# Optimization experiments

Measured on AMD Instinct MI355X. Metric: run time of the kernel, lower is better.

Reference implementation:

```python
import jax, jax.numpy as jnp
import numpy as np

H, W, HID = 7, 7, 512
IN_DIM = 1024

def _grid_edges(h, w):
    e = []
    for r in range(h):
        for c in range(w):
            n = r * w + c
            if c < w - 1:
                e.append((n, n + 1))
            if r < h - 1:
                e.append((n, n + w))
    return np.asarray(e, dtype=np.int32).T  # [2, 84]

_BASE = _grid_edges(H, W)

def setup_inputs() -> dict:
    key = jax.random.key(0)
    ks = jax.random.split(key, 16)
    B = 1024
    s = 0.02
    return {
        "visual_feat": jax.random.normal(ks[0], (B, 512, H, W), jnp.float32),
        "tactile_feat": jax.random.normal(ks[1], (B, 512, H, W), jnp.float32),
        "proj_W": jax.random.normal(ks[2], (IN_DIM, 2), jnp.float32) * s,
        "proj_b": jnp.zeros((2,), jnp.float32),
        "gc1_rel_W": jax.random.normal(ks[3], (IN_DIM, HID), jnp.float32) * s,
        "gc1_rel_b": jnp.zeros((HID,), jnp.float32),
        "gc1_root_W": jax.random.normal(ks[4], (IN_DIM, HID), jnp.float32) * s,
        "bn1_gamma": jnp.ones((HID,), jnp.float32),
        "bn1_beta": jnp.zeros((HID,), jnp.float32),
        "gc2_rel_W": jax.random.normal(ks[5], (HID, HID), jnp.float32) * s,
        "gc2_rel_b": jnp.zeros((HID,), jnp.float32),
        "gc2_root_W": jax.random.normal(ks[6], (HID, HID), jnp.float32) * s,
        "bn2_gamma": jnp.ones((HID,), jnp.float32),
        "bn2_beta": jnp.zeros((HID,), jnp.float32),
        "dec_W": jax.random.normal(ks[7], (HID + 1, HID), jnp.float32) * s,
        "dec_b": jnp.zeros((HID,), jnp.float32),
    }

def _batched_edges(B):
    off = (np.arange(B, dtype=np.int32) * (H * W))[:, None]
    src = (_BASE[0][None, :] + off).reshape(-1)
    dst = (_BASE[1][None, :] + off).reshape(-1)
    return jnp.asarray(src), jnp.asarray(dst)

def _bn(x, gamma, beta):
    mu = x.mean(0)
    var = x.var(0)  # biased, matches torch BN normalization
    return (x - mu) * jax.lax.rsqrt(var + 1e-5) * gamma + beta

def _graph_conv(x, src, dst, ew, W_rel, b_rel, W_root, N):
    msg = ew[:, None] * x[src]                      # [E, D]
    agg = jax.ops.segment_sum(msg, dst, num_segments=N)
    deg = jax.ops.segment_sum(jnp.ones_like(ew), dst, num_segments=N)
    agg = agg / jnp.maximum(deg, 1.0)[:, None]
    return agg @ W_rel + b_rel + x @ W_root

def reference(visual_feat, tactile_feat, proj_W, proj_b,
              gc1_rel_W, gc1_rel_b, gc1_root_W, bn1_gamma, bn1_beta,
              gc2_rel_W, gc2_rel_b, gc2_root_W, bn2_gamma, bn2_beta,
              dec_W, dec_b):
    B = visual_feat.shape[0]
    N = B * H * W
    # node features: concat channels, NCHW -> N x (2C)
    node = jnp.concatenate([visual_feat, tactile_feat], axis=1)
    node = node.transpose(0, 2, 3, 1).reshape(N, IN_DIM)
    src, dst = _batched_edges(B)
    coords = node @ proj_W + proj_b                 # [N, 2]
    dist = jnp.linalg.norm(coords[src] - coords[dst], axis=1)
    edge_attr = jax.nn.sigmoid(1.0 / (dist + 1e-6))  # [E]
    alpha = jnp.exp(edge_attr)
    alpha = alpha / (alpha.sum() + 1e-8)            # global normalization over all edges
    x = jax.nn.relu(_bn(_graph_conv(node, src, dst, alpha, gc1_rel_W, gc1_rel_b, gc1_root_W, N), bn1_gamma, bn1_beta))
    x = jax.nn.relu(_bn(_graph_conv(x, src, dst, alpha, gc2_rel_W, gc2_rel_b, gc2_root_W, N), bn2_gamma, bn2_beta))
    # scatter_mean of edge_attr over both endpoints
    ids = jnp.concatenate([src, dst])
    vals = jnp.concatenate([edge_attr, edge_attr])
    nw_sum = jax.ops.segment_sum(vals, ids, num_segments=N)
    nw_cnt = jax.ops.segment_sum(jnp.ones_like(vals), ids, num_segments=N)
    node_w = nw_sum / jnp.maximum(nw_cnt, 1.0)      # [N]
    x = jax.nn.relu(jnp.concatenate([x, node_w[:, None]], axis=1) @ dec_W + dec_b)
    return x.reshape(B, H, W, HID).transpose(0, 3, 1, 2)
```

## Files before the change

### kernel.cpp

```cpp
#include <hip/hip_runtime.h>
#include <hip/hip_bf16.h>

typedef float f32x4 __attribute__((ext_vector_type(4)));
typedef short s16x8 __attribute__((ext_vector_type(8)));

#define N_NODES 50176

static __device__ __forceinline__ ushort f2bf(float x) {
    __hip_bfloat16 h = __float2bfloat16(x);
    return *reinterpret_cast<ushort*>(&h);
}
static __device__ __forceinline__ float bf2f(ushort u) {
    __hip_bfloat16 h = *reinterpret_cast<__hip_bfloat16*>(&u);
    return __bfloat162float(h);
}

__global__ void k_prep(const float* W1r, const float* W1t, const float* W2r, const float* W2t,
                       const float* decW, ushort* Bt1, ushort* Bt2, ushort* Bt3, float* decLast,
                       float* alpha_sum, float* bn_acc) {
    int idx = blockIdx.x * 256 + threadIdx.x;
    if (idx < 512 * 2048) {
        int j = idx >> 11, k = idx & 2047;
        float v = (k < 1024) ? W1r[k * 512 + j] : W1t[(k - 1024) * 512 + j];
        Bt1[idx] = f2bf(v);
    }
    if (idx < 512 * 1024) {
        int j = idx >> 10, k = idx & 1023;
        float v = (k < 512) ? W2r[k * 512 + j] : W2t[(k - 512) * 512 + j];
        Bt2[idx] = f2bf(v);
    }
    if (idx < 512 * 512) {
        int j = idx >> 9, k = idx & 511;
        Bt3[idx] = f2bf(decW[k * 512 + j]);
    }
    if (idx < 512) decLast[idx] = decW[512 * 512 + idx];
    if (idx < 2048) bn_acc[idx] = 0.f;
    if (idx == 0) alpha_sum[0] = 0.f;
}

__global__ void k_transpose(const float* vis, const float* tac, ushort* xcat1) {
    int b = blockIdx.x, tid = threadIdx.x;
    __shared__ ushort tile[128 * 50];
    for (int chunk = 0; chunk < 8; ++chunk) {
        const float* src = (chunk < 4 ? vis : tac) + ((size_t)b * 512 + (chunk & 3) * 128) * 49;
        for (int p = tid; p < 128 * 49; p += 256) {
            int d = p / 49, n = p - d * 49;
            tile[d * 50 + n] = f2bf(src[p]);
        }
        __syncthreads();
        for (int p = tid; p < 49 * 128; p += 256) {
            int n = p >> 7, d = p & 127;
            xcat1[((size_t)(b * 49 + n)) * 2048 + 1024 + chunk * 128 + d] = tile[d * 50 + n];
        }
        __syncthreads();
    }
}

__global__ void k_coords(const ushort* xcat1, const float* projW, const float* projb, float* coords) {
    __shared__ float pw[2048];
    int tid = threadIdx.x;
    for (int p = tid; p < 2048; p += 256) pw[p] = projW[p];
    __syncthreads();
    int lane = tid & 63, wave = tid >> 6;
    int n = blockIdx.x * 4 + wave;
    const ushort* row = xcat1 + (size_t)n * 2048 + 1024;
    float c0 = 0.f, c1 = 0.f;
    for (int j = 0; j < 16; ++j) {
        int d = j * 64 + lane;
        float v = bf2f(row[d]);
        c0 += v * pw[2 * d];
        c1 += v * pw[2 * d + 1];
    }
    for (int off = 32; off; off >>= 1) { c0 += __shfl_down(c0, off); c1 += __shfl_down(c1, off); }
    if (lane == 0) { coords[2 * n] = c0 + projb[0]; coords[2 * n + 1] = c1 + projb[1]; }
}

__global__ void k_edges(const float* coords, float* ew_exp, float* node_w, float* alpha_sum) {
    int b = blockIdx.x, tid = threadIdx.x;
    __shared__ float cx[49], cy[49], ea[84];
    __shared__ float wsum[2];
    if (tid < 49) { cx[tid] = coords[(b * 49 + tid) * 2]; cy[tid] = coords[(b * 49 + tid) * 2 + 1]; }
    __syncthreads();
    float ex = 0.f;
    if (tid < 84) {
        int s, d2;
        if (tid < 42) { int r = tid / 6, c = tid - r * 6; s = r * 7 + c; d2 = s + 1; }
        else { int t = tid - 42; int r = t / 7, c = t - r * 7; s = r * 7 + c; d2 = s + 7; }
        float dx = cx[s] - cx[d2], dy = cy[s] - cy[d2];
        float dist = sqrtf(dx * dx + dy * dy);
        float attr = 1.f / (1.f + expf(-(1.f / (dist + 1e-6f))));
        ea[tid] = attr;
        ex = expf(attr);
        ew_exp[b * 84 + tid] = ex;
    }
    for (int off = 32; off; off >>= 1) ex += __shfl_down(ex, off);
    if ((tid & 63) == 0) wsum[tid >> 6] = ex;
    __syncthreads();
    if (tid == 0) atomicAdd(alpha_sum, wsum[0] + wsum[1]);
    if (tid < 49) {
        int r = tid / 7, c = tid - r * 7;
        float s = 0.f; int cnt = 0;
        if (c > 0) { s += ea[r * 6 + c - 1]; cnt++; }
        if (c < 6) { s += ea[r * 6 + c]; cnt++; }
        if (r > 0) { s += ea[42 + (r - 1) * 7 + c]; cnt++; }
        if (r < 6) { s += ea[42 + r * 7 + c]; cnt++; }
        node_w[b * 49 + tid] = s / (float)cnt;
    }
}

__global__ void k_aggin(ushort* __restrict__ xcat, const float* __restrict__ ew,
                        const float* __restrict__ asum) {
    int T = blockIdx.x * 256 + threadIdx.x;
    int n = T >> 7, ch = T & 7 * 16 + 15;
    ch = T & 127;
    int b = n / 49, sp = n - b * 49;
    int r = sp / 7, c = sp - r * 7;
    float acc[8];
#pragma unroll
    for (int k = 0; k < 8; ++k) acc[k] = 0.f;
    int deg = (c > 0) + (r > 0);
    if (deg) {
        float sc = (1.f / (asum[0] + 1e-8f)) / (float)deg;
        if (c > 0) {
            float wl = ew[b * 84 + r * 6 + (c - 1)] * sc;
            s16x8 lv = *(const s16x8*)(xcat + (size_t)(n - 1) * 2048 + 1024 + ch * 8);
#pragma unroll
            for (int k = 0; k < 8; ++k) acc[k] += wl * bf2f((ushort)lv[k]);
        }
        if (r > 0) {
            float wt = ew[b * 84 + 42 + (r - 1) * 7 + c] * sc;
            s16x8 tv = *(const s16x8*)(xcat + (size_t)(n - 7) * 2048 + 1024 + ch * 8);
#pragma unroll
            for (int k = 0; k < 8; ++k) acc[k] += wt * bf2f((ushort)tv[k]);
        }
    }
    s16x8 o;
#pragma unroll
    for (int k = 0; k < 8; ++k) o[k] = (short)f2bf(acc[k]);
    *(s16x8*)(xcat + (size_t)n * 2048 + ch * 8) = o;
}

template <int EPI>
__global__ __launch_bounds__(256, 2)
void k_gemm(const ushort* __restrict__ A, const ushort* __restrict__ Bt, float* __restrict__ C,
            int K,
            const float* __restrict__ bias, float* __restrict__ bn_sum, float* __restrict__ bn_sumsq,
            const float* __restrict__ node_w, const float* __restrict__ decLast,
            const float* __restrict__ decb, float* __restrict__ out) {
    __shared__ ushort As[128 * 40];
    __shared__ ushort Bs[128 * 40];
    const int rowb = blockIdx.x >> 2, colb = blockIdx.x & 3;
    const int row0 = rowb << 7, col0 = colb << 7;
    const int tid = threadIdx.x;
    const int lane = tid & 63, wave = tid >> 6;
    const int wm = (wave & 1) << 6, wn = (wave >> 1) << 6;
    const int quad = lane >> 4, l16 = lane & 15;
    const int K8 = K >> 3;

    const uint4* Ag = (const uint4*)A;
    const uint4* Bg = (const uint4*)Bt;
    uint4* As4 = (uint4*)As;
    uint4* Bs4 = (uint4*)Bs;

    const int r0s = tid >> 2, kc = tid & 3;
    const size_t ia0 = (size_t)(row0 + r0s) * K8 + kc;
    const size_t ia1 = (size_t)(row0 + r0s + 64) * K8 + kc;
    const size_t ib0 = (size_t)(col0 + r0s) * K8 + kc;
    const size_t ib1 = (size_t)(col0 + r0s + 64) * K8 + kc;
    const int sa0 = r0s * 5 + kc, sa1 = (r0s + 64) * 5 + kc;

    f32x4 acc[4][4];
#pragma unroll
    for (int i = 0; i < 4; ++i)
#pragma unroll
        for (int j = 0; j < 4; ++j) acc[i][j] = (f32x4)0.f;

    const int nk = K >> 5;
    uint4 a0 = Ag[ia0], a1 = Ag[ia1], b0 = Bg[ib0], b1 = Bg[ib1];
    for (int kt = 0; kt < nk; ++kt) {
        As4[sa0] = a0; As4[sa1] = a1; Bs4[sa0] = b0; Bs4[sa1] = b1;
        __syncthreads();
        if (kt + 1 < nk) {
            const size_t o = (size_t)(kt + 1) * 4;
            a0 = Ag[ia0 + o]; a1 = Ag[ia1 + o]; b0 = Bg[ib0 + o]; b1 = Bg[ib1 + o];
        }
        s16x8 af[4], bf[4];
#pragma unroll
        for (int i = 0; i < 4; ++i) af[i] = *(const s16x8*)&As[(wm + i * 16 + l16) * 40 + quad * 8];
#pragma unroll
        for (int j = 0; j < 4; ++j) bf[j] = *(const s16x8*)&Bs[(wn + j * 16 + l16) * 40 + quad * 8];
#pragma unroll
        for (int i = 0; i < 4; ++i)
#pragma unroll
            for (int j = 0; j < 4; ++j)
                acc[i][j] = __builtin_amdgcn_mfma_f32_16x16x32_bf16(af[i], bf[j], acc[i][j], 0, 0, 0);
        __syncthreads();
    }

    if (EPI == 0) {
#pragma unroll
        for (int j = 0; j < 4; ++j) {
            int col = col0 + wn + j * 16 + l16;
            float bcol = bias[col];
            float s = 0.f, s2 = 0.f;
#pragma unroll
            for (int i = 0; i < 4; ++i) {
#pragma unroll
                for (int r = 0; r < 4; ++r) {
                    int m = row0 + wm + i * 16 + quad * 4 + r;
                    float v = acc[i][j][r] + bcol;
                    C[(size_t)m * 512 + col] = v;
                    s += v; s2 += v * v;
                }
            }
            s += __shfl_xor(s, 16); s += __shfl_xor(s, 32);
            s2 += __shfl_xor(s2, 16); s2 += __shfl_xor(s2, 32);
            if (quad == 0) { atomicAdd(&bn_sum[col], s); atomicAdd(&bn_sumsq[col], s2); }
        }
    } else {
#pragma unroll
        for (int i = 0; i < 4; ++i) {
#pragma unroll
            for (int j = 0; j < 4; ++j) {
#pragma unroll
                for (int r = 0; r < 4; ++r) {
                    int m = row0 + wm + i * 16 + quad * 4 + r;
                    int n = col0 + wn + j * 16 + l16;
                    float v = acc[i][j][r];
                    v += node_w[m] * decLast[n] + decb[n];
                    v = fmaxf(v, 0.f);
                    int bb = m / 49, sp = m - bb * 49;
                    out[((size_t)bb * 512 + n) * 49 + sp] = v;
                }
            }
        }
    }
}

__global__ void k_bnstat(const float* bn_sum, const float* bn_sumsq, const float* gamma, const float* beta,
                         float* scale, float* shift) {
    int d = threadIdx.x;
    const float invN = 1.f / (float)N_NODES;
    float mu = bn_sum[d] * invN;
    float var = bn_sumsq[d] * invN - mu * mu;
    float sc = gamma[d] * rsqrtf(var + 1e-5f);
    scale[d] = sc;
    shift[d] = beta[d] - mu * sc;
}

__global__ __launch_bounds__(256) void k_bnagg(const float* __restrict__ P, const float* __restrict__ ew,
                                               const float* __restrict__ asum,
                                               const float* __restrict__ scale, const float* __restrict__ shift,
                                               ushort* __restrict__ xcat) {
    int b = blockIdx.x, tid = threadIdx.x;
    __shared__ ushort xl[49 * 512];
    __shared__ float wl[49], wt[49];
    if (tid < 49) {
        int r = tid / 7, c = tid - r * 7;
        int deg = (c > 0) + (r > 0);
        float sc = deg ? (1.f / (asum[0] + 1e-8f)) / (float)deg : 0.f;
        wl[tid] = (c > 0) ? ew[b * 84 + r * 6 + (c - 1)] * sc : 0.f;
        wt[tid] = (r > 0) ? ew[b * 84 + 42 + (r - 1) * 7 + c] * sc : 0.f;
    }
    int dc = tid & 127;
    int sp0 = tid >> 7;
    float4 scl = ((const float4*)scale)[dc];
    float4 shf = ((const float4*)shift)[dc];
    for (int sp = sp0; sp < 49; sp += 2) {
        float4 v = ((const float4*)(P + ((size_t)b * 49 + sp) * 512))[dc];
        ushort4 o;
        o.x = f2bf(fmaxf(v.x * scl.x + shf.x, 0.f));
        o.y = f2bf(fmaxf(v.y * scl.y + shf.y, 0.f));
        o.z = f2bf(fmaxf(v.z * scl.z + shf.z, 0.f));
        o.w = f2bf(fmaxf(v.w * scl.w + shf.w, 0.f));
        *(ushort4*)&xl[sp * 512 + dc * 4] = o;
        ((ushort4*)(xcat + ((size_t)b * 49 + sp) * 1024 + 512))[dc] = o;
    }
    __syncthreads();
    for (int sp = sp0; sp < 49; sp += 2) {
        float a0 = 0.f, a1 = 0.f, a2 = 0.f, a3 = 0.f;
        float w1 = wl[sp], w2 = wt[sp];
        if (w1 != 0.f) {
            ushort4 u = *(const ushort4*)&xl[(sp - 1) * 512 + dc * 4];
            a0 += w1 * bf2f(u.x); a1 += w1 * bf2f(u.y); a2 += w1 * bf2f(u.z); a3 += w1 * bf2f(u.w);
        }
        if (w2 != 0.f) {
            ushort4 u = *(const ushort4*)&xl[(sp - 7) * 512 + dc * 4];
            a0 += w2 * bf2f(u.x); a1 += w2 * bf2f(u.y); a2 += w2 * bf2f(u.z); a3 += w2 * bf2f(u.w);
        }
        ushort4 o;
        o.x = f2bf(a0); o.y = f2bf(a1); o.z = f2bf(a2); o.w = f2bf(a3);
        ((ushort4*)(xcat + ((size_t)b * 49 + sp) * 1024))[dc] = o;
    }
}

__global__ void k_bnapply(const float* __restrict__ x, const float* __restrict__ scale,
                          const float* __restrict__ shift, ushort* __restrict__ xb) {
    int tid = threadIdx.x;
    size_t i = (size_t)blockIdx.x * 256 + tid;
    int dc = tid & 127;
    float4 scl = ((const float4*)scale)[dc];
    float4 shf = ((const float4*)shift)[dc];
    float4 v = ((const float4*)x)[i];
    ushort4 o;
    o.x = f2bf(fmaxf(v.x * scl.x + shf.x, 0.f));
    o.y = f2bf(fmaxf(v.y * scl.y + shf.y, 0.f));
    o.z = f2bf(fmaxf(v.z * scl.z + shf.z, 0.f));
    o.w = f2bf(fmaxf(v.w * scl.w + shf.w, 0.f));
    ((ushort4*)xb)[i] = o;
}

extern "C" void kernel_launch(void* const* d_in, const int* in_sizes, int n_in,
                              void* d_out, int out_size, void* d_ws, size_t ws_size,
                              hipStream_t stream) {
    const float* vis   = (const float*)d_in[0];
    const float* tac   = (const float*)d_in[1];
    const float* projW = (const float*)d_in[2];
    const float* projb = (const float*)d_in[3];
    const float* W1r   = (const float*)d_in[4];
    const float* b1    = (const float*)d_in[5];
    const float* W1t   = (const float*)d_in[6];
    const float* g1    = (const float*)d_in[7];
    const float* be1   = (const float*)d_in[8];
    const float* W2r   = (const float*)d_in[9];
    const float* b2    = (const float*)d_in[10];
    const float* W2t   = (const float*)d_in[11];
    const float* g2    = (const float*)d_in[12];
    const float* be2   = (const float*)d_in[13];
    const float* decW  = (const float*)d_in[14];
    const float* decb  = (const float*)d_in[15];
    float* out = (float*)d_out;

    char* p = (char*)d_ws;
    ushort* X   = (ushort*)p; p += 205520896;
    float*  P   = (float*)p;  p += 102760448;
    float* coords = (float*)p; p += 401408;
    float* ew     = (float*)p; p += 344064;
    float* nw     = (float*)p; p += 200704;
    ushort* Bt1   = (ushort*)p; p += 2097152;
    ushort* Bt2   = (ushort*)p; p += 1048576;
    ushort* Bt3   = (ushort*)p; p += 524288;
    float* decLast = (float*)p; p += 2048;
    float* asum   = (float*)p;  p += 256;
    float* bnacc  = (float*)p;  p += 4 * 512 * 4;
    float* scsh   = (float*)p;  p += 4 * 512 * 4;
    float* bn1s = bnacc, *bn1q = bnacc + 512, *bn2s = bnacc + 1024, *bn2q = bnacc + 1536;
    float* sc1 = scsh, *sh1 = scsh + 512, *sc2 = scsh + 1024, *sh2 = scsh + 1536;

    ushort* xcat1 = X;
    ushort* xcat2 = X;
    ushort* x3b   = X;

    k_prep<<<4096, 256, 0, stream>>>(W1r, W1t, W2r, W2t, decW, Bt1, Bt2, Bt3, decLast, asum, bnacc);
    k_transpose<<<1024, 256, 0, stream>>>(vis, tac, xcat1);
    k_coords<<<12544, 256, 0, stream>>>(xcat1, projW, projb, coords);
    k_edges<<<1024, 128, 0, stream>>>(coords, ew, nw, asum);
    k_aggin<<<25088, 256, 0, stream>>>(xcat1, ew, asum);

    k_gemm<0><<<392 * 4, 256, 0, stream>>>(xcat1, Bt1, P, 2048, b1, bn1s, bn1q, nullptr, nullptr, nullptr, nullptr);
    k_bnstat<<<1, 512, 0, stream>>>(bn1s, bn1q, g1, be1, sc1, sh1);
    k_bnagg<<<1024, 256, 0, stream>>>(P, ew, asum, sc1, sh1, xcat2);

    k_gemm<0><<<392 * 4, 256, 0, stream>>>(xcat2, Bt2, P, 1024, b2, bn2s, bn2q, nullptr, nullptr, nullptr, nullptr);
    k_bnstat<<<1, 512, 0, stream>>>(bn2s, bn2q, g2, be2, sc2, sh2);
    k_bnapply<<<25088, 256, 0, stream>>>(P, sc2, sh2, x3b);

    k_gemm<1><<<392 * 4, 256, 0, stream>>>(x3b, Bt3, nullptr, 512, nullptr, nullptr, nullptr, nw, decLast, decb, out);
}
```

Before: 816.9 us.

## Load GEMM tiles directly into LDS and pair transpose stores

The bf16 GEMM now loads its A and B tiles straight from global memory into LDS with global_load_lds, one 16-row chunk per wave. This replaces the staging through registers and the separate LDS stores, and the LDS tiles lose their row padding. Because the register prefetch of the next K-tile is also removed, each iteration now waits for its loads with no overlap, and the unpadded 64-byte row stride may add LDS bank conflicts on the fragment reads. The transpose kernel also writes two bf16 values per store, and a redundant channel-index expression is cleaned up.

```diff
diff --git a/kernel.cpp b/kernel.cpp
--- a/kernel.cpp
+++ b/kernel.cpp
@@ -13,6 +13,11 @@
 static __device__ __forceinline__ float bf2f(ushort u) {
     __hip_bfloat16 h = *reinterpret_cast<__hip_bfloat16*>(&u);
     return __bfloat162float(h);
+}
+
+static __device__ __forceinline__ void gload_lds16(const void* g, void* l) {
+    __builtin_amdgcn_global_load_lds((const __attribute__((address_space(1))) void*)g,
+                                     (__attribute__((address_space(3))) void*)l, 16, 0, 0);
 }
 
 __global__ void k_prep(const float* W1r, const float* W1t, const float* W2r, const float* W2t,
@@ -48,9 +53,12 @@
             tile[d * 50 + n] = f2bf(src[p]);
         }
         __syncthreads();
-        for (int p = tid; p < 49 * 128; p += 256) {
-            int n = p >> 7, d = p & 127;
-            xcat1[((size_t)(b * 49 + n)) * 2048 + 1024 + chunk * 128 + d] = tile[d * 50 + n];
+        for (int p = tid; p < 49 * 64; p += 256) {
+            int n = p >> 6, d2 = (p & 63) * 2;
+            ushort2 o;
+            o.x = tile[d2 * 50 + n];
+            o.y = tile[(d2 + 1) * 50 + n];
+            *(ushort2*)&xcat1[((size_t)(b * 49 + n)) * 2048 + 1024 + chunk * 128 + d2] = o;
         }
         __syncthreads();
     }
@@ -111,8 +119,7 @@
 __global__ void k_aggin(ushort* __restrict__ xcat, const float* __restrict__ ew,
                         const float* __restrict__ asum) {
     int T = blockIdx.x * 256 + threadIdx.x;
-    int n = T >> 7, ch = T & 7 * 16 + 15;
-    ch = T & 127;
+    int n = T >> 7, ch = T & 127;
     int b = n / 49, sp = n - b * 49;
     int r = sp / 7, c = sp - r * 7;
     float acc[8];
@@ -147,8 +154,8 @@
             const float* __restrict__ bias, float* __restrict__ bn_sum, float* __restrict__ bn_sumsq,
             const float* __restrict__ node_w, const float* __restrict__ decLast,
             const float* __restrict__ decb, float* __restrict__ out) {
-    __shared__ ushort As[128 * 40];
-    __shared__ ushort Bs[128 * 40];
+    __shared__ __align__(16) ushort As[128 * 32];
+    __shared__ __align__(16) ushort Bs[128 * 32];
     const int rowb = blockIdx.x >> 2, colb = blockIdx.x & 3;
     const int row0 = rowb << 7, col0 = colb << 7;
     const int tid = threadIdx.x;
@@ -159,15 +166,17 @@
 
     const uint4* Ag = (const uint4*)A;
     const uint4* Bg = (const uint4*)Bt;
-    uint4* As4 = (uint4*)As;
-    uint4* Bs4 = (uint4*)Bs;
-
-    const int r0s = tid >> 2, kc = tid & 3;
-    const size_t ia0 = (size_t)(row0 + r0s) * K8 + kc;
-    const size_t ia1 = (size_t)(row0 + r0s + 64) * K8 + kc;
-    const size_t ib0 = (size_t)(col0 + r0s) * K8 + kc;
-    const size_t ib1 = (size_t)(col0 + r0s + 64) * K8 + kc;
-    const int sa0 = r0s * 5 + kc, sa1 = (r0s + 64) * 5 + kc;
+
+    const int c0 = wave, c1 = wave + 4;
+    const int lrow = lane >> 2, lkc = lane & 3;
+    const size_t iA0 = (size_t)(row0 + c0 * 16 + lrow) * K8 + lkc;
+    const size_t iA1 = (size_t)(row0 + c1 * 16 + lrow) * K8 + lkc;
+    const size_t iB0 = (size_t)(col0 + c0 * 16 + lrow) * K8 + lkc;
+    const size_t iB1 = (size_t)(col0 + c1 * 16 + lrow) * K8 + lkc;
+    ushort* lA0 = As + c0 * 512;
+    ushort* lA1 = As + c1 * 512;
+    ushort* lB0 = Bs + c0 * 512;
+    ushort* lB1 = Bs + c1 * 512;
 
     f32x4 acc[4][4];
 #pragma unroll
@@ -176,19 +185,18 @@
         for (int j = 0; j < 4; ++j) acc[i][j] = (f32x4)0.f;
 
     const int nk = K >> 5;
-    uint4 a0 = Ag[ia0], a1 = Ag[ia1], b0 = Bg[ib0], b1 = Bg[ib1];
     for (int kt = 0; kt < nk; ++kt) {
-        As4[sa0] = a0; As4[sa1] = a1; Bs4[sa0] = b0; Bs4[sa1] = b1;
+        const size_t o = (size_t)kt * 4;
+        gload_lds16(Ag + iA0 + o, lA0);
+        gload_lds16(Ag + iA1 + o, lA1);
+        gload_lds16(Bg + iB0 + o, lB0);
+        gload_lds16(Bg + iB1 + o, lB1);
         __syncthreads();
-        if (kt + 1 < nk) {
-            const size_t o = (size_t)(kt + 1) * 4;
-            a0 = Ag[ia0 + o]; a1 = Ag[ia1 + o]; b0 = Bg[ib0 + o]; b1 = Bg[ib1 + o];
-        }
         s16x8 af[4], bf[4];
 #pragma unroll
-        for (int i = 0; i < 4; ++i) af[i] = *(const s16x8*)&As[(wm + i * 16 + l16) * 40 + quad * 8];
-#pragma unroll
-        for (int j = 0; j < 4; ++j) bf[j] = *(const s16x8*)&Bs[(wn + j * 16 + l16) * 40 + quad * 8];
+        for (int i = 0; i < 4; ++i) af[i] = *(const s16x8*)&As[(wm + i * 16 + l16) * 32 + quad * 8];
+#pragma unroll
+        for (int j = 0; j < 4; ++j) bf[j] = *(const s16x8*)&Bs[(wn + j * 16 + l16) * 32 + quad * 8];
 #pragma unroll
         for (int i = 0; i < 4; ++i)
 #pragma unroll
```

Measured after the change: 814.6 us. No clear change (-0.3%).
